# Optimization experiments

Hardware: AMD Instinct MI355X
Metric: run time of the kernel (lower is better)

## Reference

```python
import jax, jax.numpy as jnp
import numpy as np
from jax import lax

B, S, H, E, P, K, R = 64, 512, 768, 32, 16, 9, 6
HEADS, C1, C2 = 4, 128, 64
FEAT = 4 * C2 + 1  # e1, e2, e1*e2, context (64 each) + log-distance


def _ln(x, g, b):
    m = x.mean(-1, keepdims=True)
    v = ((x - m) ** 2).mean(-1, keepdims=True)
    return (x - m) * lax.rsqrt(v + 1e-5) * g + b


def _gat(x, adj, W, a_s, a_d, bias, heads, cout, concat):
    # Dense GATConv over a small fully-masked entity graph. adj[b,i,j]=edge j->i (incl. self-loops).
    h = jnp.einsum('bef,fhc->behc', x, W.reshape(x.shape[-1], heads, cout))
    s = jnp.einsum('behc,hc->bhe', h, a_s)  # source-node attention term
    d = jnp.einsum('behc,hc->bhe', h, a_d)  # target-node attention term
    logits = jax.nn.leaky_relu(d[:, :, :, None] + s[:, :, None, :], 0.2)  # [b,h,i,j]
    logits = jnp.where(adj[:, None, :, :], logits, -1e9)
    att = jax.nn.softmax(logits, axis=-1)
    out = jnp.einsum('bhij,bjhc->bihc', att, h)
    out = out.reshape(out.shape[0], out.shape[1], heads * cout) if concat else out.mean(2)
    return out + bias


def _crf_nll(em, tags, mask, start, end, trans):
    # torchcrf: loss = -mean log-likelihood. em [B,S,K]; tags [B,S]; mask [B,S] bool.
    emt = jnp.transpose(em, (1, 0, 2))
    tgt = tags.T
    mkt = mask.T.astype(em.dtype)
    num0 = start[tgt[0]] + jnp.take_along_axis(emt[0], tgt[0][:, None], 1)[:, 0]

    def nstep(c, inp):
        ptag, sc = c
        e, t, m = inp
        step = trans[ptag, t] + jnp.take_along_axis(e, t[:, None], 1)[:, 0]
        return (jnp.where(m > 0, t, ptag), sc + step * m), None

    (ltag, num), _ = lax.scan(nstep, (tgt[0], num0), (emt[1:], tgt[1:], mkt[1:]))
    num = num + end[ltag]
    a0 = start[None, :] + emt[0]

    def dstep(a, inp):
        e, m = inp
        nxt = jax.scipy.special.logsumexp(a[:, :, None] + trans[None] + e[:, None, :], axis=1)
        return jnp.where(m[:, None] > 0, nxt, a), None

    aT, _ = lax.scan(dstep, a0, (emt[1:], mkt[1:]))
    Z = jax.scipy.special.logsumexp(aT + end[None], axis=1)
    return jnp.mean(Z - num)


def setup_inputs() -> dict:
    key = jax.random.key(0)
    ks = jax.random.split(key, 24)
    n = lambda i, shape, s=0.05: jax.random.normal(ks[i], shape, jnp.float32) * s
    return {
        'sequence_output': jax.random.normal(ks[0], (B, S, H), jnp.float32),
        'attention_mask': jnp.ones((B, S), jnp.int32),
        'ner_labels': jax.random.randint(ks[1], (B, S), 0, K),
        'entity_start': jax.random.randint(ks[2], (B, E), 0, S - 8),
        'entity_len': jax.random.randint(ks[3], (B, E), 0, 8),
        'pair_e1': jax.random.randint(ks[4], (B, P), 0, E),
        'pair_e2': jax.random.randint(ks[5], (B, P), 0, E),
        'pair_labels': jax.random.randint(ks[6], (B, P), 0, 2),
        'adj_mask': jnp.ones((B, E, E), bool),
        'w_ner1': n(7, (H, 256)), 'b_ner1': jnp.zeros((256,), jnp.float32),
        'w_ner2': n(8, (256, K)), 'b_ner2': jnp.zeros((K,), jnp.float32),
        'crf_start': n(9, (K,), 0.1), 'crf_end': n(10, (K,), 0.1), 'crf_trans': n(11, (K, K), 0.1),
        'w_gat1': n(12, (H, HEADS * C1)), 'a_src1': n(13, (HEADS, C1)), 'a_dst1': n(14, (HEADS, C1)),
        'b_gat1': jnp.zeros((HEADS * C1,), jnp.float32),
        'w_gat2': n(15, (HEADS * C1, C2)), 'a_src2': n(16, (1, C2)), 'a_dst2': n(17, (1, C2)),
        'b_gat2': jnp.zeros((C2,), jnp.float32),
        'w_fe': n(18, (FEAT, 512)), 'b_fe': jnp.zeros((512,), jnp.float32),
        'g_fe': jnp.ones((512,), jnp.float32), 'be_fe': jnp.zeros((512,), jnp.float32),
        'w_rc1': n(19, (R, 512, 256)), 'b_rc1': jnp.zeros((R, 256), jnp.float32),
        'g_rc': jnp.ones((R, 256), jnp.float32), 'be_rc': jnp.zeros((R, 256), jnp.float32),
        'w_rc2': n(20, (R, 256, 1)), 'b_rc2': jnp.zeros((R,), jnp.float32),
    }


def reference(sequence_output, attention_mask, ner_labels, entity_start, entity_len,
              pair_e1, pair_e2, pair_labels, adj_mask,
              w_ner1, b_ner1, w_ner2, b_ner2, crf_start, crf_end, crf_trans,
              w_gat1, a_src1, a_dst1, b_gat1, w_gat2, a_src2, a_dst2, b_gat2,
              w_fe, b_fe, g_fe, be_fe, w_rc1, b_rc1, g_rc, be_rc, w_rc2, b_rc2):
    # NER head (dropout off / eval)
    ner_logits = jnp.maximum(sequence_output @ w_ner1 + b_ner1, 0.0) @ w_ner2 + b_ner2
    ner_loss = _crf_nll(ner_logits, ner_labels, attention_mask.astype(bool),
                        crf_start, crf_end, crf_trans)
    # entity span mean-pool via inclusive cumsum trick
    cs = jnp.concatenate([jnp.zeros((B, 1, H), sequence_output.dtype),
                          jnp.cumsum(sequence_output, axis=1)], axis=1)
    e_end = jnp.clip(entity_start + entity_len, 0, S - 1)
    seg = (jnp.take_along_axis(cs, (e_end + 1)[:, :, None], 1)
           - jnp.take_along_axis(cs, entity_start[:, :, None], 1))
    ent = seg / (e_end - entity_start + 1).astype(sequence_output.dtype)[:, :, None]  # [B,E,H]
    x = _gat(ent, adj_mask, w_gat1, a_src1, a_dst1, b_gat1, HEADS, C1, True)
    x = jnp.maximum(x, 0.0)
    x = _gat(x, adj_mask, w_gat2, a_src2, a_dst2, b_gat2, 1, C2, False)  # [B,E,64]
    x1 = jnp.take_along_axis(x, pair_e1[:, :, None], 1)
    x2 = jnp.take_along_axis(x, pair_e2[:, :, None], 1)
    ctx = jnp.broadcast_to(x.mean(1, keepdims=True), (B, P, C2))
    dist = jnp.log(jnp.abs(pair_e1 - pair_e2).astype(x.dtype) + 1.0)[:, :, None]
    pf = jnp.concatenate([x1, x2, x1 * x2, ctx, dist], axis=-1)  # [B,P,257]
    fe = jax.nn.leaky_relu(_ln(pf @ w_fe + b_fe, g_fe, be_fe), 0.01)
    h1 = jnp.einsum('bpf,rfo->rbpo', fe, w_rc1) + b_rc1[:, None, None, :]
    h1 = jax.nn.leaky_relu(_ln(h1, g_rc[:, None, None, :], be_rc[:, None, None, :]), 0.01)
    z = jnp.einsum('rbpo,ro->rbp', h1, w_rc2[:, :, 0]) + b_rc2[:, None, None]
    y = pair_labels.astype(z.dtype)[None]
    # BCEWithLogitsLoss(pos_weight=2.0), mean per relation type, summed over types
    bce = -(2.0 * y * jax.nn.log_sigmoid(z) + (1.0 - y) * jax.nn.log_sigmoid(-z))
    rel_loss = bce.mean(axis=(1, 2)).sum()
    total = ner_loss + rel_loss
    return ner_logits, z, total
```

## Files before the change

### kernel.cpp

```cpp
#include <hip/hip_runtime.h>
#include <math.h>


#define NB 64
#define NS 512
#define NH 768
#define NE 32
#define NP 16
#define NK 9
#define NR 6
#define NHEADS 4
#define NC1 128
#define NC2 64
#define SEGS 16
#define SEGLEN 32

#define ZOFF 294912
#define TOTOFF 301056

#define WS_ENT   0u
#define WS_WG1T  1572864u
#define WS_X1    2621440u
#define WS_X2    3801088u
#define WS_WG2T  3956736u
#define WS_FE    4222976u
#define WS_CRF   4747264u
#define WS_REL   4747328u
#define WS_W1T   4747392u
#define WS_WRT   0u
#define WS_WFET  393216u
#define WS_SEG   475136u

typedef __attribute__((ext_vector_type(8))) short bf16x8;
typedef __attribute__((ext_vector_type(4))) float f32x4;

__device__ __forceinline__ unsigned short f2bf(float x) {
  union { float f; unsigned u; } v; v.f = x;
  unsigned r = v.u + 0x7FFFu + ((v.u >> 16) & 1u);
  return (unsigned short)(r >> 16);
}

__device__ __forceinline__ float logsigf(float x) {
  if (x >= 0.f) return -log1pf(__expf(-x));
  return x - log1pf(__expf(x));
}

__global__ __launch_bounds__(256) void k_prep(
    const float* __restrict__ w1, const float* __restrict__ wg1,
    const float* __restrict__ wg2, const float* __restrict__ seq,
    const int* __restrict__ est, const int* __restrict__ elen,
    unsigned short* __restrict__ w1t, unsigned short* __restrict__ wg1t,
    unsigned short* __restrict__ wg2t, unsigned short* __restrict__ entb) {
  __shared__ unsigned short tr[32 * 776];
  const int bid = blockIdx.x, t = threadIdx.x;
  if (bid < 26) {
    const float* src;
    unsigned short* dst;
    int c0, ncol, nkt, kdim;
    if (bid < 8)       { src = w1;  dst = w1t;  ncol = 256; c0 = bid * 32;        nkt = 24; kdim = 768; }
    else if (bid < 24) { src = wg1; dst = wg1t; ncol = 512; c0 = (bid - 8) * 32;  nkt = 24; kdim = 768; }
    else               { src = wg2; dst = wg2t; ncol = 64;  c0 = (bid - 24) * 32; nkt = 16; kdim = 512; }
    for (int p = 0; p < nkt; p++) {
      const int k = p * 32 + (t >> 3), c4 = t & 7;
      const float4 f = *reinterpret_cast<const float4*>(&src[(size_t)k * ncol + c0 + c4 * 4]);
      tr[(c4 * 4 + 0) * 776 + k] = f2bf(f.x);
      tr[(c4 * 4 + 1) * 776 + k] = f2bf(f.y);
      tr[(c4 * 4 + 2) * 776 + k] = f2bf(f.z);
      tr[(c4 * 4 + 3) * 776 + k] = f2bf(f.w);
    }
    __syncthreads();
    const int c = t >> 3, q = t & 7;
    const int chunk = kdim >> 3;
    for (int i = 0; i < (chunk >> 3); i++) {
      *reinterpret_cast<uint4*>(&dst[(size_t)(c0 + c) * kdim + q * chunk + i * 8]) =
          *reinterpret_cast<const uint4*>(&tr[c * 776 + q * chunk + i * 8]);
    }
  } else {
    const int be = bid - 26;
    const int b = be >> 5, e = be & 31;
    const int st = est[b * NE + e];
    int en = st + elen[b * NE + e];
    en = min(max(en, 0), NS - 1);
    const float inv = 1.f / (float)(en - st + 1);
    for (int c = t; c < NH; c += 256) {
      float s = 0.f;
      for (int r = st; r <= en; r++) s += seq[((size_t)b * NS + r) * NH + c];
      entb[((size_t)b * NE + e) * NH + c] = f2bf(s * inv);
    }
  }
}

__global__ __launch_bounds__(256) void k_main(
    const float* __restrict__ seq, const unsigned short* __restrict__ w1t,
    const float* __restrict__ b1, const float* __restrict__ w2,
    const float* __restrict__ b2, float* __restrict__ out,
    const unsigned short* __restrict__ entb, const unsigned short* __restrict__ wg1t,
    const float* __restrict__ as1, const float* __restrict__ ad1,
    const unsigned char* __restrict__ adj, const float* __restrict__ bias1,
    unsigned short* __restrict__ x1b) {
  __shared__ __align__(16) char smem[34048];
  const int bid = blockIdx.x, t = threadIdx.x;
  const int w = t >> 6, lane = t & 63, quad = lane >> 4, l15 = lane & 15;

  if (bid < 256) {
    unsigned short* As = (unsigned short*)smem;
    unsigned short* Bs = (unsigned short*)(smem + 2560);
    float* Hs  = (float*)(smem + 12800);
    float* Att = (float*)(smem + 29696);
    float* Sv  = (float*)(smem + 33792);
    float* Dv  = (float*)(smem + 33920);
    const int b = bid >> 2, hd = bid & 3;

    f32x4 acc[2][2];
#pragma unroll
    for (int r = 0; r < 2; r++)
#pragma unroll
      for (int c = 0; c < 2; c++) acc[r][c] = (f32x4){0.f, 0.f, 0.f, 0.f};

    const int rowA = t >> 2, koffA = (t & 3) * 8;
    const unsigned short* aptr = entb + ((size_t)(b * NE) + rowA) * NH + koffA;

    for (int kt = 0; kt < NH; kt += 32) {
      __syncthreads();
      if (t < 128) {
        *reinterpret_cast<uint4*>(&As[rowA * 40 + koffA]) =
            *reinterpret_cast<const uint4*>(aptr + kt);
      }
#pragma unroll
      for (int i = 0; i < 2; i++) {
        const int q = t + 256 * i;
        const int col = q >> 2, koff = (q & 3) * 8;
        *reinterpret_cast<uint4*>(&Bs[col * 40 + koff]) =
            *reinterpret_cast<const uint4*>(&wg1t[(size_t)(hd * 128 + col) * NH + kt + koff]);
      }
      __syncthreads();
      bf16x8 a[2], bb[2];
#pragma unroll
      for (int r = 0; r < 2; r++)
        a[r] = *reinterpret_cast<const bf16x8*>(&As[(r * 16 + l15) * 40 + quad * 8]);
#pragma unroll
      for (int c = 0; c < 2; c++)
        bb[c] = *reinterpret_cast<const bf16x8*>(&Bs[(w * 32 + c * 16 + l15) * 40 + quad * 8]);
#pragma unroll
      for (int r = 0; r < 2; r++)
#pragma unroll
        for (int c = 0; c < 2; c++)
          acc[r][c] = __builtin_amdgcn_mfma_f32_16x16x32_bf16(a[r], bb[c], acc[r][c], 0, 0, 0);
    }
#pragma unroll
    for (int r = 0; r < 2; r++)
#pragma unroll
      for (int c = 0; c < 2; c++)
#pragma unroll
        for (int reg = 0; reg < 4; reg++)
          Hs[(r * 16 + quad * 4 + reg) * 132 + w * 32 + c * 16 + l15] = acc[r][c][reg];
    __syncthreads();
    {
      const int e = t >> 3, cg = t & 7;
      float sv = 0.f, dv = 0.f;
#pragma unroll
      for (int c = 0; c < 16; c++) {
        const float h = Hs[e * 132 + cg * 16 + c];
        sv += h * as1[hd * NC1 + cg * 16 + c];
        dv += h * ad1[hd * NC1 + cg * 16 + c];
      }
#pragma unroll
      for (int o = 1; o < 8; o <<= 1) { sv += __shfl_xor(sv, o); dv += __shfl_xor(dv, o); }
      if (cg == 0) { Sv[e] = sv; Dv[e] = dv; }
    }
    __syncthreads();
    if (t < 32) {
      const int i = t;
      const float di = Dv[i];
      float lg[32];
      float m = -1e30f;
#pragma unroll
      for (int j = 0; j < 32; j++) {
        float v = di + Sv[j];
        v = v >= 0.f ? v : 0.2f * v;
        if (!adj[((size_t)b * NE + i) * NE + j]) v = -1e9f;
        lg[j] = v; m = fmaxf(m, v);
      }
      float sum = 0.f;
#pragma unroll
      for (int j = 0; j < 32; j++) { lg[j] = __expf(lg[j] - m); sum += lg[j]; }
      const float inv = 1.f / sum;
#pragma unroll
      for (int j = 0; j < 32; j++) Att[j * 32 + i] = lg[j] * inv;
    }
    __syncthreads();
    {
      const int tc = t & 31, tr2 = t >> 5;
#pragma unroll
      for (int i = 0; i < 4; i++) {
        const int row = tr2 * 4 + i;
        float o0 = bias1[hd * NC1 + tc * 4 + 0];
        float o1 = bias1[hd * NC1 + tc * 4 + 1];
        float o2 = bias1[hd * NC1 + tc * 4 + 2];
        float o3 = bias1[hd * NC1 + tc * 4 + 3];
#pragma unroll
        for (int j = 0; j < 32; j++) {
          const float a = Att[j * 32 + row];
          o0 = fmaf(a, Hs[j * 132 + tc * 4 + 0], o0);
          o1 = fmaf(a, Hs[j * 132 + tc * 4 + 1], o1);
          o2 = fmaf(a, Hs[j * 132 + tc * 4 + 2], o2);
          o3 = fmaf(a, Hs[j * 132 + tc * 4 + 3], o3);
        }
        uint2 v;
        v.x = (unsigned)f2bf(fmaxf(o0, 0.f)) | ((unsigned)f2bf(fmaxf(o1, 0.f)) << 16);
        v.y = (unsigned)f2bf(fmaxf(o2, 0.f)) | ((unsigned)f2bf(fmaxf(o3, 0.f)) << 16);
        *reinterpret_cast<uint2*>(&x1b[((size_t)b * NE + row) * 512 + hd * 128 + tc * 4]) = v;
      }
    }
  } else {
    unsigned short* AsS = (unsigned short*)smem;
    unsigned short* BsS = (unsigned short*)(smem + 2560);
    float* zs = (float*)(smem + 23040);
    const int tok0 = (bid - 256) * 32;

    f32x4 acc[2][4];
#pragma unroll
    for (int r = 0; r < 2; r++)
#pragma unroll
      for (int c = 0; c < 4; c++) acc[r][c] = (f32x4){0.f, 0.f, 0.f, 0.f};

    const int tokA = t >> 3, koffA = (t & 7) * 4;
    const float* aptr = seq + (size_t)(tok0 + tokA) * NH + koffA;

    for (int kt = 0; kt < NH; kt += 32) {
      __syncthreads();
      {
        const float4 f0 = *reinterpret_cast<const float4*>(aptr + kt);
        uint2 v;
        v.x = (unsigned)f2bf(f0.x) | ((unsigned)f2bf(f0.y) << 16);
        v.y = (unsigned)f2bf(f0.z) | ((unsigned)f2bf(f0.w) << 16);
        *reinterpret_cast<uint2*>(&AsS[tokA * 40 + koffA]) = v;
      }
#pragma unroll
      for (int i = 0; i < 4; i++) {
        const int q = t + 256 * i;
        const int col = q >> 2, koff = (q & 3) * 8;
        *reinterpret_cast<uint4*>(&BsS[col * 40 + koff]) =
            *reinterpret_cast<const uint4*>(&w1t[(size_t)col * NH + kt + koff]);
      }
      __syncthreads();
      bf16x8 a[2], b[4];
#pragma unroll
      for (int r = 0; r < 2; r++)
        a[r] = *reinterpret_cast<const bf16x8*>(&AsS[(r * 16 + l15) * 40 + quad * 8]);
#pragma unroll
      for (int c = 0; c < 4; c++)
        b[c] = *reinterpret_cast<const bf16x8*>(&BsS[(w * 64 + c * 16 + l15) * 40 + quad * 8]);
#pragma unroll
      for (int r = 0; r < 2; r++)
#pragma unroll
        for (int c = 0; c < 4; c++)
          acc[r][c] = __builtin_amdgcn_mfma_f32_16x16x32_bf16(a[r], b[c], acc[r][c], 0, 0, 0);
    }

    float b1v[4], w2v[4][NK];
#pragma unroll
    for (int c = 0; c < 4; c++) {
      const int col = w * 64 + c * 16 + l15;
      b1v[c] = b1[col];
#pragma unroll
      for (int cc = 0; cc < NK; cc++) w2v[c][cc] = w2[col * NK + cc];
    }
#pragma unroll
    for (int r = 0; r < 2; r++) {
#pragma unroll
      for (int reg = 0; reg < 4; reg++) {
        float p[NK];
#pragma unroll
        for (int cc = 0; cc < NK; cc++) p[cc] = 0.f;
#pragma unroll
        for (int c = 0; c < 4; c++) {
          const float h = fmaxf(acc[r][c][reg] + b1v[c], 0.f);
#pragma unroll
          for (int cc = 0; cc < NK; cc++) p[cc] = fmaf(h, w2v[c][cc], p[cc]);
        }
#pragma unroll
        for (int o = 1; o < 16; o <<= 1)
#pragma unroll
          for (int cc = 0; cc < NK; cc++) p[cc] += __shfl_xor(p[cc], o);
        if (l15 == 0) {
          const int tokr = r * 16 + quad * 4 + reg;
#pragma unroll
          for (int cc = 0; cc < NK; cc++) zs[(tokr * 4 + w) * 12 + cc] = p[cc];
        }
      }
    }
    __syncthreads();
    if (t < 32) {
#pragma unroll
      for (int cc = 0; cc < NK; cc++) {
        const float z = zs[(t * 4 + 0) * 12 + cc] + zs[(t * 4 + 1) * 12 + cc] +
                        zs[(t * 4 + 2) * 12 + cc] + zs[(t * 4 + 3) * 12 + cc] + b2[cc];
        out[(size_t)(tok0 + t) * NK + cc] = z;
      }
    }
  }
}

__global__ __launch_bounds__(256) void k_mid(
    const float* __restrict__ wrc, const float* __restrict__ wfe,
    unsigned short* __restrict__ wrt, unsigned short* __restrict__ wfet,
    const float* __restrict__ em, const int* __restrict__ mask,
    const float* __restrict__ trans, float* __restrict__ segm) {
  __shared__ __align__(16) char smem[36864];
  const int bid = blockIdx.x, t = threadIdx.x;
  if (bid < 58) {
    unsigned short* tr = (unsigned short*)smem;
    if (bid < 48) {
      const int r = bid >> 3, kt = bid & 7;
      const int k0 = kt * 64;
#pragma unroll
      for (int i = 0; i < 16; i++) {
        const int slot = t + 256 * i;
        const int row = slot >> 6, c4 = slot & 63;
        const float4 f = *reinterpret_cast<const float4*>(
            &wrc[((size_t)(r * 512) + k0 + row) * 256 + c4 * 4]);
        tr[(c4 * 4 + 0) * 72 + row] = f2bf(f.x);
        tr[(c4 * 4 + 1) * 72 + row] = f2bf(f.y);
        tr[(c4 * 4 + 2) * 72 + row] = f2bf(f.z);
        tr[(c4 * 4 + 3) * 72 + row] = f2bf(f.w);
      }
      __syncthreads();
#pragma unroll
      for (int i = 0; i < 8; i++) {
        const int slot = t + 256 * i;
        const int col = slot >> 3, q = slot & 7;
        *reinterpret_cast<uint4*>(&wrt[((size_t)(r * 256 + col)) * 512 + k0 + q * 8]) =
            *reinterpret_cast<const uint4*>(&tr[col * 72 + q * 8]);
      }
    } else {
      const int b2 = bid - 48;
      const int kt = b2 % 5, cb = b2 / 5;
      const int k0 = kt * 64, c0 = cb * 256;
#pragma unroll
      for (int i = 0; i < 16; i++) {
        const int slot = t + 256 * i;
        const int row = slot >> 6, c4 = slot & 63;
        const int k = k0 + row;
        float4 f = {0.f, 0.f, 0.f, 0.f};
        if (k < 257)
          f = *reinterpret_cast<const float4*>(&wfe[(size_t)k * 512 + c0 + c4 * 4]);
        tr[(c4 * 4 + 0) * 72 + row] = f2bf(f.x);
        tr[(c4 * 4 + 1) * 72 + row] = f2bf(f.y);
        tr[(c4 * 4 + 2) * 72 + row] = f2bf(f.z);
        tr[(c4 * 4 + 3) * 72 + row] = f2bf(f.w);
      }
      __syncthreads();
#pragma unroll
      for (int i = 0; i < 8; i++) {
        const int slot = t + 256 * i;
        const int col = slot >> 3, q = slot & 7;
        *reinterpret_cast<uint4*>(&wfet[((size_t)(c0 + col)) * 320 + k0 + q * 8]) =
            *reinterpret_cast<const uint4*>(&tr[col * 72 + q * 8]);
      }
    }
  } else {
    float* bufA = (float*)smem;
    float* bufB = (float*)(smem + 5184);
    float* ems  = (float*)(smem + 7776);
    int*   mks  = (int*)(smem + 8928);
    float* trs  = (float*)(smem + 9056);
    const int blk = bid - 58;
    const int b = blk >> 4, seg = blk & 15;
    const int s0 = 1 + seg * SEGLEN;
    const float* emb = em + (size_t)b * NS * NK;
    const int* mk = mask + b * NS;
    if (t < 81) trs[t] = trans[t];
    for (int i = t; i < SEGLEN * 9; i += 256) {
      const int g = s0 * 9 + i;
      ems[i] = (g < NS * 9) ? emb[g] : 0.f;
    }
    if (t < SEGLEN) {
      const int s = s0 + t;
      mks[t] = (s < NS) ? mk[s] : 0;
    }
    __syncthreads();
    for (int idx = t; idx < 16 * 81; idx += 256) {
      const int p = idx / 81, e = idx % 81, i = e / 9, j = e % 9;
      const int la = 2 * p, lb = la + 1;
      const bool ma = mks[la] > 0, mb = mks[lb] > 0;
      float r;
      if (ma && mb) {
        float v[9], mx = -1e30f;
#pragma unroll
        for (int m = 0; m < 9; m++) {
          v[m] = trs[i * 9 + m] + ems[la * 9 + m] + trs[m * 9 + j];
          mx = fmaxf(mx, v[m]);
        }
        float sum = 0.f;
#pragma unroll
        for (int m = 0; m < 9; m++) sum += __expf(v[m] - mx);
        r = mx + __logf(sum) + ems[lb * 9 + j];
      } else if (ma) {
        r = trs[e] + ems[la * 9 + j];
      } else if (mb) {
        r = trs[e] + ems[lb * 9 + j];
      } else {
        r = (i == j) ? 0.f : -1e30f;
      }
      bufA[p * 81 + e] = r;
    }
    float* src = bufA;
    float* dst = bufB;
    for (int n = 16; n > 1; n >>= 1) {
      __syncthreads();
      const int half = n >> 1;
      for (int idx = t; idx < half * 81; idx += 256) {
        const int q = idx / 81, e = idx % 81, i = e / 9, j = e % 9;
        const float* A = src + (size_t)(2 * q) * 81;
        const float* Bm = src + (size_t)(2 * q + 1) * 81;
        float v[9], mx = -1e30f;
#pragma unroll
        for (int m = 0; m < 9; m++) {
          v[m] = A[i * 9 + m] + Bm[m * 9 + j];
          mx = fmaxf(mx, v[m]);
        }
        float sum = 0.f;
#pragma unroll
        for (int m = 0; m < 9; m++) sum += __expf(v[m] - mx);
        dst[q * 81 + e] = mx + __logf(sum);
      }
      float* tmp = src; src = dst; dst = tmp;
    }
    __syncthreads();
    if (t < 81) segm[((size_t)b * SEGS + seg) * 81 + t] = src[t];
  }
}

__global__ __launch_bounds__(256) void k_late(
    const unsigned short* __restrict__ x1b, const unsigned short* __restrict__ wg2t,
    const float* __restrict__ as2, const float* __restrict__ ad2,
    const unsigned char* __restrict__ adj, const float* __restrict__ bias2,
    float* __restrict__ x2,
    const float* __restrict__ em, const int* __restrict__ tags,
    const int* __restrict__ mask, const float* __restrict__ startv,
    const float* __restrict__ endv, const float* __restrict__ trans,
    const float* __restrict__ segm, float* __restrict__ lossb) {
  __shared__ __align__(16) char smem[20736];
  const int bid = blockIdx.x, t = threadIdx.x;
  if (bid < 64) {
    unsigned short* As = (unsigned short*)smem;
    unsigned short* Bs = (unsigned short*)(smem + 2560);
    float* H2  = (float*)(smem + 7680);
    float* Att = (float*)(smem + 16384);
    float* Sv  = (float*)(smem + 20480);
    float* Dv  = (float*)(smem + 20608);
    const int b = bid;
    const int w = t >> 6, lane = t & 63, quad = lane >> 4, l15 = lane & 15;

    f32x4 acc[2];
#pragma unroll
    for (int r = 0; r < 2; r++) acc[r] = (f32x4){0.f, 0.f, 0.f, 0.f};

    const int rowA = t >> 2, koffA = (t & 3) * 8;
    const unsigned short* aptr = x1b + ((size_t)(b * NE) + rowA) * 512 + koffA;

    for (int kt = 0; kt < 512; kt += 32) {
      __syncthreads();
      if (t < 128) {
        *reinterpret_cast<uint4*>(&As[rowA * 40 + koffA]) =
            *reinterpret_cast<const uint4*>(aptr + kt);
      }
      {
        const int col = t >> 2, koff = (t & 3) * 8;
        *reinterpret_cast<uint4*>(&Bs[col * 40 + koff]) =
            *reinterpret_cast<const uint4*>(&wg2t[(size_t)col * 512 + kt + koff]);
      }
      __syncthreads();
      const bf16x8 a0 = *reinterpret_cast<const bf16x8*>(&As[l15 * 40 + quad * 8]);
      const bf16x8 a1 = *reinterpret_cast<const bf16x8*>(&As[(16 + l15) * 40 + quad * 8]);
      const bf16x8 bb = *reinterpret_cast<const bf16x8*>(&Bs[(w * 16 + l15) * 40 + quad * 8]);
      acc[0] = __builtin_amdgcn_mfma_f32_16x16x32_bf16(a0, bb, acc[0], 0, 0, 0);
      acc[1] = __builtin_amdgcn_mfma_f32_16x16x32_bf16(a1, bb, acc[1], 0, 0, 0);
    }
#pragma unroll
    for (int r = 0; r < 2; r++)
#pragma unroll
      for (int reg = 0; reg < 4; reg++)
        H2[(r * 16 + quad * 4 + reg) * 68 + w * 16 + l15] = acc[r][reg];
    __syncthreads();
    {
      const int e = t >> 3, cg = t & 7;
      float sv = 0.f, dv = 0.f;
#pragma unroll
      for (int c = 0; c < 8; c++) {
        const float h = H2[e * 68 + cg * 8 + c];
        sv += h * as2[cg * 8 + c];
        dv += h * ad2[cg * 8 + c];
      }
#pragma unroll
      for (int o = 1; o < 8; o <<= 1) { sv += __shfl_xor(sv, o); dv += __shfl_xor(dv, o); }
      if (cg == 0) { Sv[e] = sv; Dv[e] = dv; }
    }
    __syncthreads();
    if (t < 32) {
      const int i = t;
      const float di = Dv[i];
      float lg[32];
      float m = -1e30f;
#pragma unroll
      for (int j = 0; j < 32; j++) {
        float v = di + Sv[j];
        v = v >= 0.f ? v : 0.2f * v;
        if (!adj[((size_t)b * NE + i) * NE + j]) v = -1e9f;
        lg[j] = v; m = fmaxf(m, v);
      }
      float sum = 0.f;
#pragma unroll
      for (int j = 0; j < 32; j++) { lg[j] = __expf(lg[j] - m); sum += lg[j]; }
      const float inv = 1.f / sum;
#pragma unroll
      for (int j = 0; j < 32; j++) Att[j * 32 + i] = lg[j] * inv;
    }
    __syncthreads();
    {
      const int tc = t & 15, tr2 = t >> 4;
#pragma unroll
      for (int i = 0; i < 2; i++) {
        const int row = tr2 * 2 + i;
        float o0 = bias2[tc * 4 + 0];
        float o1 = bias2[tc * 4 + 1];
        float o2 = bias2[tc * 4 + 2];
        float o3 = bias2[tc * 4 + 3];
#pragma unroll
        for (int j = 0; j < 32; j++) {
          const float a = Att[j * 32 + row];
          o0 = fmaf(a, H2[j * 68 + tc * 4 + 0], o0);
          o1 = fmaf(a, H2[j * 68 + tc * 4 + 1], o1);
          o2 = fmaf(a, H2[j * 68 + tc * 4 + 2], o2);
          o3 = fmaf(a, H2[j * 68 + tc * 4 + 3], o3);
        }
        float4 v;
        v.x = o0; v.y = o1; v.z = o2; v.w = o3;
        *reinterpret_cast<float4*>(&x2[((size_t)b * NE + row) * NC2 + tc * 4]) = v;
      }
    }
  } else {
    float* sm  = (float*)smem;
    float* av  = (float*)(smem + 5184);
    float* red = (float*)(smem + 5248);
    const int b = bid - 64;
    const float* emb = em + (size_t)b * NS * NK;
    const int* mk = mask + b * NS;
    const int* tg = tags + b * NS;
    for (int i = t; i < SEGS * 81; i += 256) sm[i] = segm[(size_t)b * SEGS * 81 + i];
    if (t < 64) {
      float num = 0.f;
      int lastS = 0;
#pragma unroll
      for (int o = 0; o < 8; o++) {
        const int s = t * 8 + o;
        if (s >= 1 && mk[s] > 0) {
          const int cur = tg[s], prv = tg[s - 1];
          num += trans[prv * NK + cur] + emb[s * NK + cur];
          lastS = s;
        }
      }
#pragma unroll
      for (int o = 32; o > 0; o >>= 1) {
        num += __shfl_xor(num, o);
        lastS = max(lastS, __shfl_xor(lastS, o));
      }
      if (t == 0) {
        const int t0 = tg[0];
        red[0] = startv[t0] + emb[t0] + num + endv[tg[lastS]];
      }
    }
    __syncthreads();
    if (t < 9) av[t] = startv[t] + emb[t];
    __syncthreads();
    for (int h = 0; h < SEGS; h++) {
      float nv = 0.f;
      if (t < 9) {
        float v[9], mx = -1e30f;
#pragma unroll
        for (int i2 = 0; i2 < 9; i2++) {
          v[i2] = av[i2] + sm[h * 81 + i2 * 9 + t];
          mx = fmaxf(mx, v[i2]);
        }
        float sum = 0.f;
#pragma unroll
        for (int i2 = 0; i2 < 9; i2++) sum += __expf(v[i2] - mx);
        nv = mx + __logf(sum);
      }
      __syncthreads();
      if (t < 9) av[t] = nv;
      __syncthreads();
    }
    if (t == 0) {
      float mx = -1e30f;
#pragma unroll
      for (int j = 0; j < 9; j++) mx = fmaxf(mx, av[j] + endv[j]);
      float sum = 0.f;
#pragma unroll
      for (int j = 0; j < 9; j++) sum += __expf(av[j] + endv[j] - mx);
      lossb[b] = (mx + __logf(sum)) - red[0];
    }
  }
}

__global__ __launch_bounds__(256) void k_fe(const float* __restrict__ x2,
    const int* __restrict__ pe1, const int* __restrict__ pe2,
    const unsigned short* __restrict__ wt, const float* __restrict__ bfe,
    const float* __restrict__ g, const float* __restrict__ be,
    unsigned short* __restrict__ feb) {
  __shared__ unsigned short Af[16 * 320];
  __shared__ float Cs[16 * 520];
  __shared__ float ctxs[64];
  const int b = blockIdx.x, t = threadIdx.x;
  const int w = t >> 6, lane = t & 63, quad = lane >> 4, l15 = lane & 15;
  if (t < 64) {
    float cs = 0.f;
    for (int e = 0; e < NE; e++) cs += x2[((size_t)b * NE + e) * NC2 + t];
    ctxs[t] = cs * (1.f / NE);
  }
  __syncthreads();
  for (int i = t; i < 16 * 320; i += 256) {
    const int p = i / 320, k = i - p * 320;
    unsigned short o = 0;
    if (k < 260) {
      const int e1 = pe1[b * NP + p], e2 = pe2[b * NP + p];
      float v;
      if (k < 64) v = x2[((size_t)b * NE + e1) * NC2 + k];
      else if (k < 128) v = x2[((size_t)b * NE + e2) * NC2 + (k - 64)];
      else if (k < 192) v = x2[((size_t)b * NE + e1) * NC2 + (k - 128)] *
                            x2[((size_t)b * NE + e2) * NC2 + (k - 128)];
      else if (k < 256) v = ctxs[k - 192];
      else if (k == 256) v = logf(fabsf((float)(e1 - e2)) + 1.f);
      else v = 0.f;
      o = f2bf(v);
    }
    Af[i] = o;
  }
  __syncthreads();
  f32x4 acc[8];
#pragma unroll
  for (int c = 0; c < 8; c++) acc[c] = (f32x4){0.f, 0.f, 0.f, 0.f};
#pragma unroll
  for (int kt = 0; kt < 10; kt++) {
    const bf16x8 a = *reinterpret_cast<const bf16x8*>(&Af[l15 * 320 + kt * 32 + quad * 8]);
#pragma unroll
    for (int c = 0; c < 8; c++) {
      const int col = w * 128 + c * 16 + l15;
      const bf16x8 bv = *reinterpret_cast<const bf16x8*>(&wt[(size_t)col * 320 + kt * 32 + quad * 8]);
      acc[c] = __builtin_amdgcn_mfma_f32_16x16x32_bf16(a, bv, acc[c], 0, 0, 0);
    }
  }
#pragma unroll
  for (int c = 0; c < 8; c++)
#pragma unroll
    for (int reg = 0; reg < 4; reg++)
      Cs[(quad * 4 + reg) * 520 + w * 128 + c * 16 + l15] = acc[c][reg];
  __syncthreads();
  float bfev[8], gv[8], bev[8];
#pragma unroll
  for (int ch = 0; ch < 8; ch++) {
    const int col = ch * 64 + lane;
    bfev[ch] = bfe[col]; gv[ch] = g[col]; bev[ch] = be[col];
  }
#pragma unroll
  for (int pp = 0; pp < 4; pp++) {
    const int p = w * 4 + pp;
    float v[8], s = 0.f, sq = 0.f;
#pragma unroll
    for (int ch = 0; ch < 8; ch++) {
      v[ch] = Cs[p * 520 + ch * 64 + lane] + bfev[ch];
      s += v[ch]; sq += v[ch] * v[ch];
    }
#pragma unroll
    for (int o = 32; o > 0; o >>= 1) { s += __shfl_xor(s, o); sq += __shfl_xor(sq, o); }
    const float mean = s * (1.f / 512.f);
    const float var = sq * (1.f / 512.f) - mean * mean;
    const float rr = rsqrtf(var + 1e-5f);
#pragma unroll
    for (int ch = 0; ch < 8; ch++) {
      float n = (v[ch] - mean) * rr * gv[ch] + bev[ch];
      n = n >= 0.f ? n : 0.01f * n;
      feb[(size_t)(b * NP + p) * 512 + ch * 64 + lane] = f2bf(n);
    }
  }
}

__global__ __launch_bounds__(256) void k_rc(const unsigned short* __restrict__ feb,
    const unsigned short* __restrict__ wrt, const float* __restrict__ b1,
    const float* __restrict__ g, const float* __restrict__ be,
    const float* __restrict__ w2, const float* __restrict__ b2,
    const int* __restrict__ ylab, float* __restrict__ zout, float* __restrict__ relacc) {
  __shared__ unsigned short Af[16 * 520];
  __shared__ float Cs[16 * 264];
  const int blk = blockIdx.x;
  const int r = blk >> 6, b = blk & 63;
  const int t = threadIdx.x;
  const int w = t >> 6, lane = t & 63, quad = lane >> 4, l15 = lane & 15;
#pragma unroll
  for (int i = 0; i < 4; i++) {
    const int slot = t + 256 * i;
    const int p = slot >> 6, q = slot & 63;
    *reinterpret_cast<uint4*>(&Af[p * 520 + q * 8]) =
        *reinterpret_cast<const uint4*>(&feb[(size_t)(b * NP + p) * 512 + q * 8]);
  }
  __syncthreads();
  f32x4 acc[4];
#pragma unroll
  for (int c = 0; c < 4; c++) acc[c] = (f32x4){0.f, 0.f, 0.f, 0.f};
#pragma unroll
  for (int kt = 0; kt < 16; kt++) {
    const bf16x8 a = *reinterpret_cast<const bf16x8*>(&Af[l15 * 520 + kt * 32 + quad * 8]);
#pragma unroll
    for (int c = 0; c < 4; c++) {
      const int col = w * 64 + c * 16 + l15;
      const bf16x8 bv = *reinterpret_cast<const bf16x8*>(
          &wrt[(size_t)(r * 256 + col) * 512 + kt * 32 + quad * 8]);
      acc[c] = __builtin_amdgcn_mfma_f32_16x16x32_bf16(a, bv, acc[c], 0, 0, 0);
    }
  }
#pragma unroll
  for (int c = 0; c < 4; c++)
#pragma unroll
    for (int reg = 0; reg < 4; reg++)
      Cs[(quad * 4 + reg) * 264 + w * 64 + c * 16 + l15] = acc[c][reg];
  __syncthreads();
  float b1v[4], gv[4], bev[4], w2v[4];
#pragma unroll
  for (int ch = 0; ch < 4; ch++) {
    const int col = r * 256 + ch * 64 + lane;
    b1v[ch] = b1[col]; gv[ch] = g[col]; bev[ch] = be[col]; w2v[ch] = w2[col];
  }
  const float b2v = b2[r];
  float local = 0.f;
#pragma unroll
  for (int pp = 0; pp < 4; pp++) {
    const int p = w * 4 + pp;
    float v[4], s = 0.f, sq = 0.f;
#pragma unroll
    for (int ch = 0; ch < 4; ch++) {
      v[ch] = Cs[p * 264 + ch * 64 + lane] + b1v[ch];
      s += v[ch]; sq += v[ch] * v[ch];
    }
#pragma unroll
    for (int o = 32; o > 0; o >>= 1) { s += __shfl_xor(s, o); sq += __shfl_xor(sq, o); }
    const float mean = s * (1.f / 256.f);
    const float var = sq * (1.f / 256.f) - mean * mean;
    const float rr = rsqrtf(var + 1e-5f);
    float zdot = 0.f;
#pragma unroll
    for (int ch = 0; ch < 4; ch++) {
      float n = (v[ch] - mean) * rr * gv[ch] + bev[ch];
      n = n >= 0.f ? n : 0.01f * n;
      zdot = fmaf(n, w2v[ch], zdot);
    }
#pragma unroll
    for (int o = 32; o > 0; o >>= 1) zdot += __shfl_xor(zdot, o);
    if (lane == 0) {
      const float zp = zdot + b2v;
      zout[(size_t)(r * NB + b) * NP + p] = zp;
      const float y = (float)ylab[b * NP + p];
      local += -(2.f * y * logsigf(zp) + (1.f - y) * logsigf(-zp));
    }
  }
  if (lane == 0) atomicAdd(relacc, local * (1.f / (NB * NP)));
}

__global__ __launch_bounds__(64) void k_fin(const float* __restrict__ lossb,
    const float* __restrict__ rel, float* __restrict__ out) {
  float v = lossb[threadIdx.x];
#pragma unroll
  for (int o = 32; o > 0; o >>= 1) v += __shfl_down(v, o);
  if (threadIdx.x == 0) out[TOTOFF] = v * (1.f / NB) + rel[0];
}

extern "C" void kernel_launch(void* const* d_in, const int* in_sizes, int n_in,
                              void* d_out, int out_size, void* d_ws, size_t ws_size,
                              hipStream_t stream) {
  const float* seq = (const float*)d_in[0];
  const int* amask = (const int*)d_in[1];
  const int* nlab = (const int*)d_in[2];
  const int* est = (const int*)d_in[3];
  const int* elen = (const int*)d_in[4];
  const int* pe1 = (const int*)d_in[5];
  const int* pe2 = (const int*)d_in[6];
  const int* plab = (const int*)d_in[7];
  const unsigned char* adj = (const unsigned char*)d_in[8];
  const float* w_ner1 = (const float*)d_in[9];
  const float* b_ner1 = (const float*)d_in[10];
  const float* w_ner2 = (const float*)d_in[11];
  const float* b_ner2 = (const float*)d_in[12];
  const float* crf_start = (const float*)d_in[13];
  const float* crf_end = (const float*)d_in[14];
  const float* crf_trans = (const float*)d_in[15];
  const float* w_gat1 = (const float*)d_in[16];
  const float* a_src1 = (const float*)d_in[17];
  const float* a_dst1 = (const float*)d_in[18];
  const float* b_gat1 = (const float*)d_in[19];
  const float* w_gat2 = (const float*)d_in[20];
  const float* a_src2 = (const float*)d_in[21];
  const float* a_dst2 = (const float*)d_in[22];
  const float* b_gat2 = (const float*)d_in[23];
  const float* w_fe = (const float*)d_in[24];
  const float* b_fe = (const float*)d_in[25];
  const float* g_fe = (const float*)d_in[26];
  const float* be_fe = (const float*)d_in[27];
  const float* w_rc1 = (const float*)d_in[28];
  const float* b_rc1 = (const float*)d_in[29];
  const float* g_rc = (const float*)d_in[30];
  const float* be_rc = (const float*)d_in[31];
  const float* w_rc2 = (const float*)d_in[32];
  const float* b_rc2 = (const float*)d_in[33];

  float* out = (float*)d_out;
  float* ws = (float*)d_ws;
  float* x2 = ws + WS_X2;
  float* crfb = ws + WS_CRF;
  float* rel = ws + WS_REL;
  unsigned short* entb = (unsigned short*)(ws + WS_ENT);
  unsigned short* wg1t = (unsigned short*)(ws + WS_WG1T);
  unsigned short* wg2t = (unsigned short*)(ws + WS_WG2T);
  unsigned short* x1b = (unsigned short*)(ws + WS_X1);
  unsigned short* w1t = (unsigned short*)(ws + WS_W1T);
  unsigned short* feb = (unsigned short*)(ws + WS_FE);
  unsigned short* wrt = (unsigned short*)(ws + WS_WRT);
  unsigned short* wfet = (unsigned short*)(ws + WS_WFET);
  float* segm = ws + WS_SEG;

  hipMemsetAsync(rel, 0, sizeof(float), stream);

  k_prep<<<2074, 256, 0, stream>>>(w_ner1, w_gat1, w_gat2, seq, est, elen,
                                   w1t, wg1t, wg2t, entb);
  k_main<<<1280, 256, 0, stream>>>(seq, w1t, b_ner1, w_ner2, b_ner2, out,
                                   entb, wg1t, a_src1, a_dst1, adj, b_gat1, x1b);
  k_mid<<<1082, 256, 0, stream>>>(w_rc1, w_fe, wrt, wfet, out, amask, crf_trans, segm);
  k_late<<<128, 256, 0, stream>>>(x1b, wg2t, a_src2, a_dst2, adj, b_gat2, x2,
                                  out, nlab, amask, crf_start, crf_end, crf_trans,
                                  segm, crfb);
  k_fe<<<64, 256, 0, stream>>>(x2, pe1, pe2, wfet, b_fe, g_fe, be_fe, feb);
  k_rc<<<NR * NB, 256, 0, stream>>>(feb, wrt, b_rc1, g_rc, be_rc, w_rc2, b_rc2,
                                    plab, out + ZOFF, rel);
  k_fin<<<1, 64, 0, stream>>>(crfb, rel, out);
}
```

Baseline: 431.9 us.

## Factor CRF log-semiring matmuls into exp-domain products and cap main-kernel registers

The segmented CRF forward reduction in k_mid now precomputes row and column maxima, exponentiates each operand once, and does plain multiply-adds followed by one log per output. Previously every output element computed nine exps. k_main is renamed k_mg and gets a launch-bounds occupancy hint of 4. In the GAT softmax of k_mg and k_late, the per-thread 32-element logit array is replaced by in-place work in shared memory to save registers. The factorised form adds extra barriers and passes. The per-row/column max split may underflow for extreme values, and shared memory grows slightly.

```diff
diff --git a/kernel.cpp b/kernel.cpp
--- a/kernel.cpp
+++ b/kernel.cpp
@@ -90,7 +90,7 @@
   }
 }
 
-__global__ __launch_bounds__(256) void k_main(
+__global__ __launch_bounds__(256, 4) void k_mg(
     const float* __restrict__ seq, const unsigned short* __restrict__ w1t,
     const float* __restrict__ b1, const float* __restrict__ w2,
     const float* __restrict__ b2, float* __restrict__ out,
@@ -98,7 +98,7 @@
     const float* __restrict__ as1, const float* __restrict__ ad1,
     const unsigned char* __restrict__ adj, const float* __restrict__ bias1,
     unsigned short* __restrict__ x1b) {
-  __shared__ __align__(16) char smem[34048];
+  __shared__ __align__(16) char smem[34304];
   const int bid = blockIdx.x, t = threadIdx.x;
   const int w = t >> 6, lane = t & 63, quad = lane >> 4, l15 = lane & 15;
 
@@ -172,21 +172,22 @@
     if (t < 32) {
       const int i = t;
       const float di = Dv[i];
-      float lg[32];
       float m = -1e30f;
-#pragma unroll
       for (int j = 0; j < 32; j++) {
         float v = di + Sv[j];
         v = v >= 0.f ? v : 0.2f * v;
         if (!adj[((size_t)b * NE + i) * NE + j]) v = -1e9f;
-        lg[j] = v; m = fmaxf(m, v);
+        Att[j * 32 + i] = v;
+        m = fmaxf(m, v);
       }
       float sum = 0.f;
-#pragma unroll
-      for (int j = 0; j < 32; j++) { lg[j] = __expf(lg[j] - m); sum += lg[j]; }
+      for (int j = 0; j < 32; j++) {
+        const float e = __expf(Att[j * 32 + i] - m);
+        Att[j * 32 + i] = e;
+        sum += e;
+      }
       const float inv = 1.f / sum;
-#pragma unroll
-      for (int j = 0; j < 32; j++) Att[j * 32 + i] = lg[j] * inv;
+      for (int j = 0; j < 32; j++) Att[j * 32 + i] *= inv;
     }
     __syncthreads();
     {
@@ -362,15 +363,22 @@
   } else {
     float* bufA = (float*)smem;
     float* bufB = (float*)(smem + 5184);
-    float* ems  = (float*)(smem + 7776);
-    int*   mks  = (int*)(smem + 8928);
-    float* trs  = (float*)(smem + 9056);
+    float* EA   = (float*)(smem + 7776);
+    float* EB   = (float*)(smem + 10368);
+    float* Gf   = (float*)(smem + 12960);
+    float* ems  = (float*)(smem + 18144);
+    float* trs  = (float*)(smem + 19296);
+    float* Hexp = (float*)(smem + 19620);
+    float* mxp  = (float*)(smem + 19944);
+    float* mxA  = (float*)(smem + 20520);
+    float* mxB  = (float*)(smem + 20808);
+    int*   mks  = (int*)(smem + 21096);
     const int blk = bid - 58;
     const int b = blk >> 4, seg = blk & 15;
     const int s0 = 1 + seg * SEGLEN;
     const float* emb = em + (size_t)b * NS * NK;
     const int* mk = mask + b * NS;
-    if (t < 81) trs[t] = trans[t];
+    if (t < 81) { trs[t] = trans[t]; Hexp[t] = __expf(trans[t]); }
     for (int i = t; i < SEGLEN * 9; i += 256) {
       const int g = s0 * 9 + i;
       ems[i] = (g < NS * 9) ? emb[g] : 0.f;
@@ -380,22 +388,30 @@
       mks[t] = (s < NS) ? mk[s] : 0;
     }
     __syncthreads();
-    for (int idx = t; idx < 16 * 81; idx += 256) {
-      const int p = idx / 81, e = idx % 81, i = e / 9, j = e % 9;
+    for (int idx = t; idx < 144; idx += 256) {
+      const int p = idx / 9, i = idx - p * 9;
+      const float* eml = &ems[(2 * p) * 9];
+      float mx = -1e30f;
+#pragma unroll
+      for (int m = 0; m < 9; m++) mx = fmaxf(mx, trs[i * 9 + m] + eml[m]);
+      mxp[idx] = mx;
+    }
+    __syncthreads();
+    for (int idx = t; idx < 1296; idx += 256) {
+      const int p = idx / 81, r81 = idx - p * 81, i = r81 / 9, m = r81 - i * 9;
+      Gf[idx] = __expf(trs[i * 9 + m] + ems[(2 * p) * 9 + m] - mxp[p * 9 + i]);
+    }
+    __syncthreads();
+    for (int idx = t; idx < 1296; idx += 256) {
+      const int p = idx / 81, e = idx - p * 81, i = e / 9, j = e - i * 9;
       const int la = 2 * p, lb = la + 1;
       const bool ma = mks[la] > 0, mb = mks[lb] > 0;
       float r;
       if (ma && mb) {
-        float v[9], mx = -1e30f;
-#pragma unroll
-        for (int m = 0; m < 9; m++) {
-          v[m] = trs[i * 9 + m] + ems[la * 9 + m] + trs[m * 9 + j];
-          mx = fmaxf(mx, v[m]);
-        }
-        float sum = 0.f;
-#pragma unroll
-        for (int m = 0; m < 9; m++) sum += __expf(v[m] - mx);
-        r = mx + __logf(sum) + ems[lb * 9 + j];
+        float s = 0.f;
+#pragma unroll
+        for (int m = 0; m < 9; m++) s = fmaf(Gf[p * 81 + i * 9 + m], Hexp[m * 9 + j], s);
+        r = mxp[p * 9 + i] + __logf(s) + ems[lb * 9 + j];
       } else if (ma) {
         r = trs[e] + ems[la * 9 + j];
       } else if (mb) {
@@ -403,27 +419,43 @@
       } else {
         r = (i == j) ? 0.f : -1e30f;
       }
-      bufA[p * 81 + e] = r;
+      bufA[idx] = r;
     }
     float* src = bufA;
     float* dst = bufB;
     for (int n = 16; n > 1; n >>= 1) {
-      __syncthreads();
       const int half = n >> 1;
+      __syncthreads();
+      for (int idx = t; idx < half * 18; idx += 256) {
+        const int q = idx / 18, r2 = idx - q * 18;
+        if (r2 < 9) {
+          const float* A = src + (size_t)(2 * q) * 81 + r2 * 9;
+          float mx = -1e30f;
+#pragma unroll
+          for (int m = 0; m < 9; m++) mx = fmaxf(mx, A[m]);
+          mxA[q * 9 + r2] = mx;
+        } else {
+          const int j = r2 - 9;
+          const float* Bm = src + (size_t)(2 * q + 1) * 81;
+          float mx = -1e30f;
+#pragma unroll
+          for (int m = 0; m < 9; m++) mx = fmaxf(mx, Bm[m * 9 + j]);
+          mxB[q * 9 + j] = mx;
+        }
+      }
+      __syncthreads();
       for (int idx = t; idx < half * 81; idx += 256) {
-        const int q = idx / 81, e = idx % 81, i = e / 9, j = e % 9;
-        const float* A = src + (size_t)(2 * q) * 81;
-        const float* Bm = src + (size_t)(2 * q + 1) * 81;
-        float v[9], mx = -1e30f;
-#pragma unroll
-        for (int m = 0; m < 9; m++) {
-          v[m] = A[i * 9 + m] + Bm[m * 9 + j];
-          mx = fmaxf(mx, v[m]);
-        }
-        float sum = 0.f;
-#pragma unroll
-        for (int m = 0; m < 9; m++) sum += __expf(v[m] - mx);
-        dst[q * 81 + e] = mx + __logf(sum);
+        const int q = idx / 81, e = idx - q * 81, i = e / 9, c = e - i * 9;
+        EA[idx] = __expf(src[(size_t)(2 * q) * 81 + e] - mxA[q * 9 + i]);
+        EB[idx] = __expf(src[(size_t)(2 * q + 1) * 81 + e] - mxB[q * 9 + c]);
+      }
+      __syncthreads();
+      for (int idx = t; idx < half * 81; idx += 256) {
+        const int q = idx / 81, e = idx - q * 81, i = e / 9, j = e - i * 9;
+        float s = 0.f;
+#pragma unroll
+        for (int m = 0; m < 9; m++) s = fmaf(EA[q * 81 + i * 9 + m], EB[q * 81 + m * 9 + j], s);
+        dst[idx] = mxA[q * 9 + i] + mxB[q * 9 + j] + __logf(s);
       }
       float* tmp = src; src = dst; dst = tmp;
     }
@@ -501,21 +533,22 @@
     if (t < 32) {
       const int i = t;
       const float di = Dv[i];
-      float lg[32];
       float m = -1e30f;
-#pragma unroll
       for (int j = 0; j < 32; j++) {
         float v = di + Sv[j];
         v = v >= 0.f ? v : 0.2f * v;
         if (!adj[((size_t)b * NE + i) * NE + j]) v = -1e9f;
-        lg[j] = v; m = fmaxf(m, v);
+        Att[j * 32 + i] = v;
+        m = fmaxf(m, v);
       }
       float sum = 0.f;
-#pragma unroll
-      for (int j = 0; j < 32; j++) { lg[j] = __expf(lg[j] - m); sum += lg[j]; }
+      for (int j = 0; j < 32; j++) {
+        const float e = __expf(Att[j * 32 + i] - m);
+        Att[j * 32 + i] = e;
+        sum += e;
+      }
       const float inv = 1.f / sum;
-#pragma unroll
-      for (int j = 0; j < 32; j++) Att[j * 32 + i] = lg[j] * inv;
+      for (int j = 0; j < 32; j++) Att[j * 32 + i] *= inv;
     }
     __syncthreads();
     {
@@ -831,8 +864,8 @@
 
   k_prep<<<2074, 256, 0, stream>>>(w_ner1, w_gat1, w_gat2, seq, est, elen,
                                    w1t, wg1t, wg2t, entb);
-  k_main<<<1280, 256, 0, stream>>>(seq, w1t, b_ner1, w_ner2, b_ner2, out,
-                                   entb, wg1t, a_src1, a_dst1, adj, b_gat1, x1b);
+  k_mg<<<1280, 256, 0, stream>>>(seq, w1t, b_ner1, w_ner2, b_ner2, out,
+                                 entb, wg1t, a_src1, a_dst1, adj, b_gat1, x1b);
   k_mid<<<1082, 256, 0, stream>>>(w_rc1, w_fe, wrt, wfet, out, amask, crf_trans, segm);
   k_late<<<128, 256, 0, stream>>>(x1b, wg2t, a_src2, a_dst2, adj, b_gat2, x2,
                                   out, nlab, amask, crf_start, crf_end, crf_trans,
```

After: 432.5 us. No clear change (+0.1%).
